# Performance work log

Hardware: AMD Instinct MI355X
Metric: run time of the kernel (lower is better)

Reference implementation:

```python
import jax, jax.numpy as jnp
import numpy as np

FEAT_DIM = 256
DEPTH = 2
N = 8192


def setup_inputs() -> dict:
    key = jax.random.key(0)
    ks = jax.random.split(key, 5)
    bd = 1.0 / FEAT_DIM
    X = jax.random.normal(ks[0], (N, FEAT_DIM), dtype=jnp.float32)
    coefs = jax.random.normal(ks[1], (N,), dtype=jnp.float32)
    linear = jax.random.uniform(ks[2], (DEPTH, FEAT_DIM), minval=-bd, maxval=bd, dtype=jnp.float32)
    dirv = jax.random.uniform(ks[3], (DEPTH, FEAT_DIM), minval=-bd, maxval=bd, dtype=jnp.float32)
    feat = jax.random.uniform(ks[4], (DEPTH, FEAT_DIM), minval=-bd, maxval=bd, dtype=jnp.float32)
    return {"X": X, "coefs": coefs, "linear": linear, "dirv": dirv, "feat": feat}


def reference(X, coefs, linear, dirv, feat):
    # coefs is unused: the torch forward returns before the coef_embed branch.
    emb = X
    n = X.shape[0]
    for i in range(linear.shape[0]):  # depth: small fixed loop
        # torch: emb3[j,a,k] = linear[a]*emb[j,k]; q = sum_a feat[a]*emb3 = (feat.linear)*emb
        a = jnp.dot(feat[i], linear[i])
        b = jnp.dot(dirv[i], linear[i])
        q = a * emb                      # [N, F]
        k = b * emb                      # [N, F]
        k_norm = k / jnp.linalg.norm(k)  # global Frobenius norm, as torch.norm(k)
        inner = jnp.sum(q * k_norm, axis=-1)            # [N]
        scale = jnp.where(inner <= 0, inner, 0.0)       # inner * (inner<=0)
        emb = q - scale[:, None] * k_norm
        # graph_block: X_up[i] = X[i] + (X@X[i]) @ (X - X[i]) / N
        # == X + (S@X - rowsum(S)*X)/N with S = X X^T
        S = emb @ emb.T                                 # [N, N]
        emb = emb + (S @ emb - jnp.sum(S, axis=1, keepdims=True) * emb) / n
    out = jnp.mean(emb @ emb.T, axis=-1)[:-1]           # [N-1]
    return out
```

## Files before the change

kernel.cpp:

```cpp
#include <hip/hip_runtime.h>
#include <math.h>

constexpr int NROW = 8192;
constexpr int FD   = 256;
constexpr int NZ   = 16;

typedef unsigned short u16;
typedef __attribute__((ext_vector_type(8))) short short8;
typedef __attribute__((ext_vector_type(4))) float f32x4;


__device__ __forceinline__ float f_of(float nj, float A, float B, float AB) {
    float inner = AB * nj;
    return A - (inner <= 0.f ? inner : 0.f) * B;
}
__device__ __forceinline__ float wred(float s) {
    #pragma unroll
    for (int off = 32; off; off >>= 1) s += __shfl_xor(s, off);
    return s;
}
__device__ __forceinline__ float dot4(float4 a, float4 b) {
    return a.x*b.x + a.y*b.y + a.z*b.z + a.w*b.w;
}
__device__ __forceinline__ u16 f2bf(float x) {
    unsigned int u = __float_as_uint(x);
    u = (u + 0x7FFFu + ((u >> 16) & 1u)) >> 16;
    return (u16)u;
}

__global__ void k_norm(const float* __restrict__ in, float* __restrict__ nrm,
                       float* __restrict__ fpart) {
    __shared__ float bs[4];
    int wave = threadIdx.x >> 6, lane = threadIdx.x & 63;
    int row = blockIdx.x * 4 + wave;
    const float4 v = *(const float4*)&in[(size_t)row * FD + lane * 4];
    float s = wred(dot4(v, v));
    if (lane == 0) { nrm[row] = s; bs[wave] = s; }
    __syncthreads();
    if (threadIdx.x == 0) fpart[blockIdx.x] = bs[0] + bs[1] + bs[2] + bs[3];
}

__global__ void __launch_bounds__(256, 2)
k_prep(const float* __restrict__ X, const float* __restrict__ nrm0,
       const float* __restrict__ fpart, const float* __restrict__ linear,
       const float* __restrict__ dirv, const float* __restrict__ feat,
       float* __restrict__ scal, float* __restrict__ f0,
       u16* __restrict__ Rbf, u16* __restrict__ Rt, float* __restrict__ cpart) {
    __shared__ u16 T[64][264];
    __shared__ float cred[4][256];
    __shared__ float l[256];
    __shared__ float ff[64];
    __shared__ float sdot[4];
    const int tid = threadIdx.x;
    const int r0 = blockIdx.x * 64;
    if (tid < 64) {
        for (int i = 0; i < 2; ++i) {
            float pa = 0.f, pb = 0.f;
            for (int k = tid; k < FD; k += 64) {
                float ll = linear[i*FD + k];
                pa += feat[i*FD + k] * ll;
                pb += dirv[i*FD + k] * ll;
            }
            pa = wred(pa); pb = wred(pb);
            if (tid == 0) { sdot[i] = pa; sdot[2 + i] = pb; }
        }
    }
    float s = 0.f;
    #pragma unroll
    for (int k = 0; k < 8; ++k) s += fpart[tid + k * 256];
    l[tid] = s;
    __syncthreads();
    for (int off = 128; off; off >>= 1) {
        if (tid < off) l[tid] += l[tid + off];
        __syncthreads();
    }
    const float F2 = l[0];
    const float a = sdot[0], b = sdot[2];
    const float sb = (b > 0.f) ? 1.f : ((b < 0.f) ? -1.f : 0.f);
    const float B = sb / sqrtf(F2);
    const float A = a, AB = a * B;
    if (blockIdx.x == 0 && tid == 0) {
        scal[0] = sdot[0]; scal[1] = sdot[1]; scal[2] = sdot[2]; scal[3] = sdot[3];
        scal[4] = A; scal[5] = B; scal[6] = AB; scal[7] = F2;
    }
    if (tid < 64) {
        float f = f_of(nrm0[r0 + tid], A, B, AB);
        ff[tid] = f;
        f0[r0 + tid] = f;
    }
    __syncthreads();
    const int cg = (tid & 63) * 4;
    const int rg = tid >> 6;
    float4 csum = make_float4(0.f, 0.f, 0.f, 0.f);
    for (int i = 0; i < 16; ++i) {
        int row = rg * 16 + i;
        float4 v = *(const float4*)&X[(size_t)(r0 + row) * FD + cg];
        float f = ff[row];
        v.x *= f; v.y *= f; v.z *= f; v.w *= f;
        csum.x += v.x; csum.y += v.y; csum.z += v.z; csum.w += v.w;
        unsigned lo = (unsigned)f2bf(v.x) | ((unsigned)f2bf(v.y) << 16);
        unsigned hi = (unsigned)f2bf(v.z) | ((unsigned)f2bf(v.w) << 16);
        uint2 pk = make_uint2(lo, hi);
        *(uint2*)&Rbf[(size_t)(r0 + row) * FD + cg] = pk;
        *(uint2*)&T[row][cg] = pk;
    }
    *(float4*)&cred[rg][cg] = csum;
    __syncthreads();
    cpart[(size_t)blockIdx.x * FD + tid] =
        cred[0][tid] + cred[1][tid] + cred[2][tid] + cred[3][tid];
    const int c = tid;
    #pragma unroll
    for (int ch = 0; ch < 8; ++ch) {
        unsigned w0 = (unsigned)T[ch*8+0][c] | ((unsigned)T[ch*8+1][c] << 16);
        unsigned w1 = (unsigned)T[ch*8+2][c] | ((unsigned)T[ch*8+3][c] << 16);
        unsigned w2 = (unsigned)T[ch*8+4][c] | ((unsigned)T[ch*8+5][c] << 16);
        unsigned w3 = (unsigned)T[ch*8+6][c] | ((unsigned)T[ch*8+7][c] << 16);
        uint4 o = make_uint4(w0, w1, w2, w3);
        *(uint4*)&Rt[(size_t)c * NROW + r0 + ch * 8] = o;
    }
}

__global__ void __launch_bounds__(256, 2)
k_gram(const u16* __restrict__ Rt, float* __restrict__ Gp) {
    const int bi = blockIdx.x, bj = blockIdx.y, z = blockIdx.z;
    const int tid = threadIdx.x, w = tid >> 6, lane = tid & 63;
    const int l15 = lane & 15, quad = lane >> 4;
    const int m0 = bi * 64 + (w & 1) * 32;
    const int n0 = bj * 64 + (w >> 1) * 32;
    const size_t kbase = (size_t)z * 512 + quad * 8;
    const u16* am0 = Rt + (size_t)(m0 + l15) * NROW + kbase;
    const u16* am1 = am0 + (size_t)16 * NROW;
    const u16* bn0 = Rt + (size_t)(n0 + l15) * NROW + kbase;
    const u16* bn1 = bn0 + (size_t)16 * NROW;
    f32x4 acc[2][2] = {};
    #pragma unroll
    for (int s = 0; s < 16; ++s) {
        int ko = s * 32;
        short8 a0 = *(const short8*)(am0 + ko);
        short8 a1 = *(const short8*)(am1 + ko);
        short8 b0 = *(const short8*)(bn0 + ko);
        short8 b1 = *(const short8*)(bn1 + ko);
        acc[0][0] = __builtin_amdgcn_mfma_f32_16x16x32_bf16(a0, b0, acc[0][0], 0, 0, 0);
        acc[0][1] = __builtin_amdgcn_mfma_f32_16x16x32_bf16(a0, b1, acc[0][1], 0, 0, 0);
        acc[1][0] = __builtin_amdgcn_mfma_f32_16x16x32_bf16(a1, b0, acc[1][0], 0, 0, 0);
        acc[1][1] = __builtin_amdgcn_mfma_f32_16x16x32_bf16(a1, b1, acc[1][1], 0, 0, 0);
    }
    float* gz = Gp + (size_t)z * (FD * FD);
    #pragma unroll
    for (int mi = 0; mi < 2; ++mi)
        #pragma unroll
        for (int ni = 0; ni < 2; ++ni)
            #pragma unroll
            for (int r = 0; r < 4; ++r)
                gz[(size_t)(m0 + mi*16 + quad*4 + r) * FD + n0 + ni*16 + l15] =
                    acc[mi][ni][r];
}

__global__ void k_gred(const float* __restrict__ Gp, u16* __restrict__ Gbf) {
    size_t e0 = (size_t)blockIdx.x * 256 + threadIdx.x;
    float s = 0.f;
    #pragma unroll
    for (int z = 0; z < NZ; ++z) s += Gp[(size_t)z * (FD * FD) + e0];
    Gbf[e0] = f2bf(s);
}

__global__ void __launch_bounds__(256, 2)
k_apply(const float* __restrict__ X, const u16* __restrict__ Rbf,
        const u16* __restrict__ Gbf, const float* __restrict__ f0,
        const float* __restrict__ cpart, float* __restrict__ emb,
        float* __restrict__ nrm1, float* __restrict__ fpart1,
        float* __restrict__ cpart1, float* __restrict__ wpart1) {
    __shared__ float Sl[32][260];
    __shared__ float csh[FD];
    __shared__ float u0s[32], ffs[32], nrs[32];
    __shared__ float nw8[32][8];
    const int tid = threadIdx.x, w = tid >> 6, lane = tid & 63;
    const int l15 = lane & 15, quad = lane >> 4;
    const int r0 = blockIdx.x * 32;

    {
        float s = 0.f;
        #pragma unroll 8
        for (int b = 0; b < 128; ++b) s += cpart[(size_t)b * FD + tid];
        csh[tid] = s;
    }
    if (tid < 32) ffs[tid] = f0[r0 + tid];
    __syncthreads();
    #pragma unroll
    for (int jj = 0; jj < 8; ++jj) {
        int row = w * 8 + jj;
        float4 xv = *(const float4*)&X[(size_t)(r0 + row) * FD + lane * 4];
        float4 cv = *(const float4*)&csh[lane * 4];
        float t = wred(dot4(xv, cv));
        if (lane == 0) u0s[row] = ffs[row] * t;
    }
    const u16* ap0 = Rbf + (size_t)(r0 + l15) * FD + quad * 8;
    const u16* ap1 = ap0 + (size_t)16 * FD;
    const int n0w = w * 64;
    const u16* bp = Gbf + (size_t)(n0w + l15) * FD + quad * 8;
    f32x4 acc[2][4] = {};
    #pragma unroll
    for (int s = 0; s < 8; ++s) {
        int ko = s * 32;
        short8 a0 = *(const short8*)(ap0 + ko);
        short8 a1 = *(const short8*)(ap1 + ko);
        short8 b0 = *(const short8*)(bp + ko);
        short8 b1 = *(const short8*)(bp + 16 * FD + ko);
        short8 b2 = *(const short8*)(bp + 32 * FD + ko);
        short8 b3 = *(const short8*)(bp + 48 * FD + ko);
        acc[0][0] = __builtin_amdgcn_mfma_f32_16x16x32_bf16(a0, b0, acc[0][0], 0, 0, 0);
        acc[0][1] = __builtin_amdgcn_mfma_f32_16x16x32_bf16(a0, b1, acc[0][1], 0, 0, 0);
        acc[0][2] = __builtin_amdgcn_mfma_f32_16x16x32_bf16(a0, b2, acc[0][2], 0, 0, 0);
        acc[0][3] = __builtin_amdgcn_mfma_f32_16x16x32_bf16(a0, b3, acc[0][3], 0, 0, 0);
        acc[1][0] = __builtin_amdgcn_mfma_f32_16x16x32_bf16(a1, b0, acc[1][0], 0, 0, 0);
        acc[1][1] = __builtin_amdgcn_mfma_f32_16x16x32_bf16(a1, b1, acc[1][1], 0, 0, 0);
        acc[1][2] = __builtin_amdgcn_mfma_f32_16x16x32_bf16(a1, b2, acc[1][2], 0, 0, 0);
        acc[1][3] = __builtin_amdgcn_mfma_f32_16x16x32_bf16(a1, b3, acc[1][3], 0, 0, 0);
    }
    #pragma unroll
    for (int mi = 0; mi < 2; ++mi)
        #pragma unroll
        for (int ni = 0; ni < 4; ++ni)
            #pragma unroll
            for (int r = 0; r < 4; ++r)
                Sl[mi*16 + quad*4 + r][n0w + ni*16 + l15] = acc[mi][ni][r];
    __syncthreads();
    const float invN = 1.0f / NROW;
    float er[32];
    float csum = 0.f;
    #pragma unroll
    for (int j = 0; j < 32; ++j) {
        float x = X[(size_t)(r0 + j) * FD + tid];
        float rv = ffs[j] * x;
        float e = rv + (Sl[j][tid] - u0s[j] * rv) * invN;
        emb[(size_t)(r0 + j) * FD + tid] = e;
        er[j] = e;
        csum += e;
        Sl[j][tid] = e * e;
    }
    __syncthreads();
    {
        int row = tid & 31, q = tid >> 5;
        float pn = 0.f;
        #pragma unroll
        for (int i = 0; i < 32; ++i) pn += Sl[row][q * 32 + i];
        nw8[row][q] = pn;
    }
    __syncthreads();
    if (tid < 32) {
        float nn = 0.f;
        #pragma unroll
        for (int q = 0; q < 8; ++q) nn += nw8[tid][q];
        nrm1[r0 + tid] = nn;
        nrs[tid] = nn;
    }
    __syncthreads();
    float wsum = 0.f;
    #pragma unroll
    for (int j = 0; j < 32; ++j) wsum += nrs[j] * er[j];
    cpart1[(size_t)blockIdx.x * FD + tid] = csum;
    wpart1[(size_t)blockIdx.x * FD + tid] = wsum;
    if (tid == 0) {
        float fp = 0.f;
        #pragma unroll
        for (int j = 0; j < 32; ++j) fp += nrs[j];
        fpart1[blockIdx.x] = fp;
    }
}

__device__ __forceinline__ void red1_scal(const float* fpart1, const float* scal,
                                          float* l, float& A, float& B, float& AB,
                                          float& kap) {
    int tid = threadIdx.x;
    l[tid] = fpart1[tid];
    __syncthreads();
    for (int off = 128; off; off >>= 1) {
        if (tid < off) l[tid] += l[tid + off];
        __syncthreads();
    }
    float F2 = l[0];
    float a = scal[1], b = scal[3];
    float sb = (b > 0.f) ? 1.f : ((b < 0.f) ? -1.f : 0.f);
    B = sb / sqrtf(F2);
    A = a; AB = a * B;
    kap = (AB <= 0.f) ? AB * B : 0.f;
    __syncthreads();
}

__global__ void k_sv(const float* __restrict__ fpart1, const float* __restrict__ scal,
                     const float* __restrict__ cpart1, const float* __restrict__ wpart1,
                     float* __restrict__ svec) {
    __shared__ float l[256];
    float A1, B1, AB1, kap;
    red1_scal(fpart1, scal, l, A1, B1, AB1, kap);
    int tid = threadIdx.x;
    int col = blockIdx.x * 4 + (tid >> 6);
    int lane = tid & 63;
    float cs = 0.f, wsm = 0.f;
    #pragma unroll
    for (int b = lane; b < 256; b += 64) {
        cs  += cpart1[(size_t)b * FD + col];
        wsm += wpart1[(size_t)b * FD + col];
    }
    #pragma unroll
    for (int off = 32; off; off >>= 1) {
        cs  += __shfl_down(cs, off);
        wsm += __shfl_down(wsm, off);
    }
    if (lane == 0) svec[col] = A1 * cs - kap * wsm;
}

__global__ void k_uv(const float* __restrict__ emb, const float* __restrict__ nrm1,
                     const float* __restrict__ scal, const float* __restrict__ fpart1,
                     const float* __restrict__ svec, float* __restrict__ u,
                     float* __restrict__ vpart) {
    __shared__ float l[256];
    __shared__ float ssh[FD];
    __shared__ float uf[16];
    float A, B, AB, kap;
    red1_scal(fpart1, scal, l, A, B, AB, kap);
    int tid = threadIdx.x;
    int r0 = blockIdx.x * 16;
    ssh[tid] = svec[tid];
    __syncthreads();
    const int wave = tid >> 6, lane = tid & 63;
    float4 sv = *(const float4*)&ssh[lane*4];
    #pragma unroll
    for (int jj = 0; jj < 4; ++jj) {
        int row = r0 + wave * 4 + jj;
        float4 ev = *(const float4*)&emb[(size_t)row * FD + lane*4];
        float s = wred(dot4(ev, sv));
        if (lane == 0) {
            float f = A - kap * nrm1[row];
            float uj = f * s;
            u[row] = uj;
            uf[wave*4 + jj] = uj * f;
        }
    }
    __syncthreads();
    float vp = 0.f;
    #pragma unroll
    for (int j = 0; j < 16; ++j)
        vp += uf[j] * emb[(size_t)(r0 + j) * FD + tid];
    vpart[(size_t)blockIdx.x * FD + tid] = vp;
}

__global__ void k_vred(const float* __restrict__ part, float* __restrict__ vec) {
    int tid = threadIdx.x;
    int col = blockIdx.x * 4 + (tid >> 6);
    int lane = tid & 63;
    float s = 0.f;
    #pragma unroll
    for (int b = 0; b < 8; ++b) s += part[(size_t)(b * 64 + lane) * FD + col];
    #pragma unroll
    for (int off = 32; off; off >>= 1) s += __shfl_down(s, off);
    if (lane == 0) vec[col] = s;
}

__global__ void k_out(const float* __restrict__ emb, const float* __restrict__ nrm1,
                      const float* __restrict__ scal, const float* __restrict__ fpart1,
                      const float* __restrict__ vvec, const float* __restrict__ u,
                      float* __restrict__ out) {
    __shared__ float l[256];
    __shared__ float vsh[FD];
    float A, B, AB, kap;
    red1_scal(fpart1, scal, l, A, B, AB, kap);
    int tid = threadIdx.x;
    int r0 = blockIdx.x * 16;
    vsh[tid] = vvec[tid];
    __syncthreads();
    const int wave = tid >> 6, lane = tid & 63;
    const float invN = 1.0f / NROW;
    float4 vv = *(const float4*)&vsh[lane*4];
    #pragma unroll
    for (int jj = 0; jj < 4; ++jj) {
        int row = r0 + wave * 4 + jj;
        float4 ev = *(const float4*)&emb[(size_t)row * FD + lane*4];
        float s = wred(dot4(ev, vv));
        if (lane == 0 && row < NROW - 1) {
            float f = A - kap * nrm1[row];
            float uj = u[row];
            out[row] = (uj + (f * s - uj * uj) * invN) * invN;
        }
    }
}

extern "C" void kernel_launch(void* const* d_in, const int* in_sizes, int n_in,
                              void* d_out, int out_size, void* d_ws, size_t ws_size,
                              hipStream_t stream) {
    const float* X      = (const float*)d_in[0];
    const float* linear = (const float*)d_in[2];
    const float* dirv   = (const float*)d_in[3];
    const float* feat   = (const float*)d_in[4];
    float* out = (float*)d_out;

    char* ws = (char*)d_ws;
    float* scal   = (float*)(ws + 0);
    float* nrm0   = (float*)(ws + 4096);
    float* nrm1   = (float*)(ws + 36864);
    float* fpart  = (float*)(ws + 69632);
    float* fpart1 = (float*)(ws + 77824);
    float* svec   = (float*)(ws + 78848);
    float* vvec   = (float*)(ws + 79872);
    float* u      = (float*)(ws + 81920);
    float* f0     = (float*)(ws + 114688);
    float* cpart  = (float*)(ws + 147456);
    u16*   Gbf    = (u16*)  (ws + 278528);
    float* cpart1 = (float*)(ws + 409600);
    float* wpart1 = (float*)(ws + 671744);
    float* vpart  = (float*)(ws + 933888);
    u16*   Rbf    = (u16*)  (ws + 2097152);
    u16*   Rt     = (u16*)  (ws + 6291456);
    float* Gp     = (float*)(ws + 10485760);
    float* emb    = (float*)(ws + 18874368);

    k_norm<<<NROW/4, 256, 0, stream>>>(X, nrm0, fpart);
    k_prep<<<128, 256, 0, stream>>>(X, nrm0, fpart, linear, dirv, feat,
                                    scal, f0, Rbf, Rt, cpart);
    k_gram<<<dim3(4,4,NZ), 256, 0, stream>>>(Rt, Gp);
    k_gred<<<256, 256, 0, stream>>>(Gp, Gbf);
    k_apply<<<256, 256, 0, stream>>>(X, Rbf, Gbf, f0, cpart, emb, nrm1,
                                     fpart1, cpart1, wpart1);
    k_sv<<<64, 256, 0, stream>>>(fpart1, scal, cpart1, wpart1, svec);
    k_uv<<<NROW/16, 256, 0, stream>>>(emb, nrm1, scal, fpart1, svec, u, vpart);
    k_vred<<<64, 256, 0, stream>>>(vpart, vvec);
    k_out<<<NROW/16, 256, 0, stream>>>(emb, nrm1, scal, fpart1, vvec, u, out);
}
```

Measured before the change: 126.0 us.

## Fuse tail kernels into cooperative grid kernel and halve row tiles

Replaces the separate k_uv, k_vred and k_out kernels with a single cooperative kernel. It keeps each block's emb rows in registers across two grid-wide syncs, so emb is read once and two launches disappear. k_prep and k_apply now use half-size row tiles with twice as many blocks, which raises parallelism. The cpart reduction is pre-reduced in k_gred so each k_apply block sums 16 partials instead of 128. The cooperative launch depends on all 512 blocks being co-resident, and grid syncs add their own latency.

```diff
diff --git a/kernel.cpp b/kernel.cpp
--- a/kernel.cpp
+++ b/kernel.cpp
@@ -1,5 +1,8 @@
 #include <hip/hip_runtime.h>
+#include <hip/hip_cooperative_groups.h>
 #include <math.h>
+
+namespace cgr = cooperative_groups;
 
 constexpr int NROW = 8192;
 constexpr int FD   = 256;
@@ -46,13 +49,13 @@
        const float* __restrict__ dirv, const float* __restrict__ feat,
        float* __restrict__ scal, float* __restrict__ f0,
        u16* __restrict__ Rbf, u16* __restrict__ Rt, float* __restrict__ cpart) {
-    __shared__ u16 T[64][264];
+    __shared__ u16 T[32][264];
     __shared__ float cred[4][256];
     __shared__ float l[256];
-    __shared__ float ff[64];
+    __shared__ float ff[32];
     __shared__ float sdot[4];
     const int tid = threadIdx.x;
-    const int r0 = blockIdx.x * 64;
+    const int r0 = blockIdx.x * 32;
     if (tid < 64) {
         for (int i = 0; i < 2; ++i) {
             float pa = 0.f, pb = 0.f;
@@ -83,34 +86,35 @@
         scal[0] = sdot[0]; scal[1] = sdot[1]; scal[2] = sdot[2]; scal[3] = sdot[3];
         scal[4] = A; scal[5] = B; scal[6] = AB; scal[7] = F2;
     }
-    if (tid < 64) {
+    if (tid < 32) {
         float f = f_of(nrm0[r0 + tid], A, B, AB);
         ff[tid] = f;
         f0[r0 + tid] = f;
     }
     __syncthreads();
-    const int cg = (tid & 63) * 4;
+    const int cg0 = (tid & 63) * 4;
     const int rg = tid >> 6;
     float4 csum = make_float4(0.f, 0.f, 0.f, 0.f);
-    for (int i = 0; i < 16; ++i) {
-        int row = rg * 16 + i;
-        float4 v = *(const float4*)&X[(size_t)(r0 + row) * FD + cg];
+    #pragma unroll
+    for (int i = 0; i < 8; ++i) {
+        int row = rg * 8 + i;
+        float4 v = *(const float4*)&X[(size_t)(r0 + row) * FD + cg0];
         float f = ff[row];
         v.x *= f; v.y *= f; v.z *= f; v.w *= f;
         csum.x += v.x; csum.y += v.y; csum.z += v.z; csum.w += v.w;
         unsigned lo = (unsigned)f2bf(v.x) | ((unsigned)f2bf(v.y) << 16);
         unsigned hi = (unsigned)f2bf(v.z) | ((unsigned)f2bf(v.w) << 16);
         uint2 pk = make_uint2(lo, hi);
-        *(uint2*)&Rbf[(size_t)(r0 + row) * FD + cg] = pk;
-        *(uint2*)&T[row][cg] = pk;
-    }
-    *(float4*)&cred[rg][cg] = csum;
+        *(uint2*)&Rbf[(size_t)(r0 + row) * FD + cg0] = pk;
+        *(uint2*)&T[row][cg0] = pk;
+    }
+    *(float4*)&cred[rg][cg0] = csum;
     __syncthreads();
     cpart[(size_t)blockIdx.x * FD + tid] =
         cred[0][tid] + cred[1][tid] + cred[2][tid] + cred[3][tid];
     const int c = tid;
     #pragma unroll
-    for (int ch = 0; ch < 8; ++ch) {
+    for (int ch = 0; ch < 4; ++ch) {
         unsigned w0 = (unsigned)T[ch*8+0][c] | ((unsigned)T[ch*8+1][c] << 16);
         unsigned w1 = (unsigned)T[ch*8+2][c] | ((unsigned)T[ch*8+3][c] << 16);
         unsigned w2 = (unsigned)T[ch*8+4][c] | ((unsigned)T[ch*8+5][c] << 16);
@@ -156,80 +160,80 @@
                     acc[mi][ni][r];
 }
 
-__global__ void k_gred(const float* __restrict__ Gp, u16* __restrict__ Gbf) {
+__global__ void k_gred(const float* __restrict__ Gp, u16* __restrict__ Gbf,
+                       const float* __restrict__ cpart, float* __restrict__ cpart2) {
     size_t e0 = (size_t)blockIdx.x * 256 + threadIdx.x;
     float s = 0.f;
     #pragma unroll
     for (int z = 0; z < NZ; ++z) s += Gp[(size_t)z * (FD * FD) + e0];
     Gbf[e0] = f2bf(s);
+    if (blockIdx.x < 16) {
+        float c = 0.f;
+        #pragma unroll
+        for (int k = 0; k < 16; ++k)
+            c += cpart[(size_t)(blockIdx.x * 16 + k) * FD + threadIdx.x];
+        cpart2[(size_t)blockIdx.x * FD + threadIdx.x] = c;
+    }
 }
 
 __global__ void __launch_bounds__(256, 2)
 k_apply(const float* __restrict__ X, const u16* __restrict__ Rbf,
         const u16* __restrict__ Gbf, const float* __restrict__ f0,
-        const float* __restrict__ cpart, float* __restrict__ emb,
+        const float* __restrict__ cpart2, float* __restrict__ emb,
         float* __restrict__ nrm1, float* __restrict__ fpart1,
         float* __restrict__ cpart1, float* __restrict__ wpart1) {
-    __shared__ float Sl[32][260];
+    __shared__ float Sl[16][260];
     __shared__ float csh[FD];
-    __shared__ float u0s[32], ffs[32], nrs[32];
-    __shared__ float nw8[32][8];
+    __shared__ float u0s[16], ffs[16], nrs[16];
+    __shared__ float nw16[16][16];
     const int tid = threadIdx.x, w = tid >> 6, lane = tid & 63;
     const int l15 = lane & 15, quad = lane >> 4;
-    const int r0 = blockIdx.x * 32;
+    const int r0 = blockIdx.x * 16;
 
     {
         float s = 0.f;
-        #pragma unroll 8
-        for (int b = 0; b < 128; ++b) s += cpart[(size_t)b * FD + tid];
+        #pragma unroll
+        for (int g = 0; g < 16; ++g) s += cpart2[(size_t)g * FD + tid];
         csh[tid] = s;
     }
-    if (tid < 32) ffs[tid] = f0[r0 + tid];
-    __syncthreads();
-    #pragma unroll
-    for (int jj = 0; jj < 8; ++jj) {
-        int row = w * 8 + jj;
+    if (tid < 16) ffs[tid] = f0[r0 + tid];
+    __syncthreads();
+    #pragma unroll
+    for (int jj = 0; jj < 4; ++jj) {
+        int row = w * 4 + jj;
         float4 xv = *(const float4*)&X[(size_t)(r0 + row) * FD + lane * 4];
         float4 cv = *(const float4*)&csh[lane * 4];
         float t = wred(dot4(xv, cv));
         if (lane == 0) u0s[row] = ffs[row] * t;
     }
-    const u16* ap0 = Rbf + (size_t)(r0 + l15) * FD + quad * 8;
-    const u16* ap1 = ap0 + (size_t)16 * FD;
+    const u16* ap = Rbf + (size_t)(r0 + l15) * FD + quad * 8;
     const int n0w = w * 64;
     const u16* bp = Gbf + (size_t)(n0w + l15) * FD + quad * 8;
-    f32x4 acc[2][4] = {};
+    f32x4 acc[4] = {};
     #pragma unroll
     for (int s = 0; s < 8; ++s) {
         int ko = s * 32;
-        short8 a0 = *(const short8*)(ap0 + ko);
-        short8 a1 = *(const short8*)(ap1 + ko);
+        short8 a0 = *(const short8*)(ap + ko);
         short8 b0 = *(const short8*)(bp + ko);
         short8 b1 = *(const short8*)(bp + 16 * FD + ko);
         short8 b2 = *(const short8*)(bp + 32 * FD + ko);
         short8 b3 = *(const short8*)(bp + 48 * FD + ko);
-        acc[0][0] = __builtin_amdgcn_mfma_f32_16x16x32_bf16(a0, b0, acc[0][0], 0, 0, 0);
-        acc[0][1] = __builtin_amdgcn_mfma_f32_16x16x32_bf16(a0, b1, acc[0][1], 0, 0, 0);
-        acc[0][2] = __builtin_amdgcn_mfma_f32_16x16x32_bf16(a0, b2, acc[0][2], 0, 0, 0);
-        acc[0][3] = __builtin_amdgcn_mfma_f32_16x16x32_bf16(a0, b3, acc[0][3], 0, 0, 0);
-        acc[1][0] = __builtin_amdgcn_mfma_f32_16x16x32_bf16(a1, b0, acc[1][0], 0, 0, 0);
-        acc[1][1] = __builtin_amdgcn_mfma_f32_16x16x32_bf16(a1, b1, acc[1][1], 0, 0, 0);
-        acc[1][2] = __builtin_amdgcn_mfma_f32_16x16x32_bf16(a1, b2, acc[1][2], 0, 0, 0);
-        acc[1][3] = __builtin_amdgcn_mfma_f32_16x16x32_bf16(a1, b3, acc[1][3], 0, 0, 0);
-    }
-    #pragma unroll
-    for (int mi = 0; mi < 2; ++mi)
-        #pragma unroll
-        for (int ni = 0; ni < 4; ++ni)
-            #pragma unroll
-            for (int r = 0; r < 4; ++r)
-                Sl[mi*16 + quad*4 + r][n0w + ni*16 + l15] = acc[mi][ni][r];
+        acc[0] = __builtin_amdgcn_mfma_f32_16x16x32_bf16(a0, b0, acc[0], 0, 0, 0);
+        acc[1] = __builtin_amdgcn_mfma_f32_16x16x32_bf16(a0, b1, acc[1], 0, 0, 0);
+        acc[2] = __builtin_amdgcn_mfma_f32_16x16x32_bf16(a0, b2, acc[2], 0, 0, 0);
+        acc[3] = __builtin_amdgcn_mfma_f32_16x16x32_bf16(a0, b3, acc[3], 0, 0, 0);
+    }
+    #pragma unroll
+    for (int ni = 0; ni < 4; ++ni)
+        #pragma unroll
+        for (int r = 0; r < 4; ++r)
+            Sl[quad*4 + r][n0w + ni*16 + l15] = acc[ni][r];
     __syncthreads();
     const float invN = 1.0f / NROW;
-    float er[32];
+    float er[16];
     float csum = 0.f;
     #pragma unroll
-    for (int j = 0; j < 32; ++j) {
+    for (int j = 0; j < 16; ++j) {
         float x = X[(size_t)(r0 + j) * FD + tid];
         float rv = ffs[j] * x;
         float e = rv + (Sl[j][tid] - u0s[j] * rv) * invN;
@@ -240,30 +244,30 @@
     }
     __syncthreads();
     {
-        int row = tid & 31, q = tid >> 5;
+        int row = tid & 15, q = tid >> 4;
         float pn = 0.f;
         #pragma unroll
-        for (int i = 0; i < 32; ++i) pn += Sl[row][q * 32 + i];
-        nw8[row][q] = pn;
-    }
-    __syncthreads();
-    if (tid < 32) {
+        for (int i = 0; i < 16; ++i) pn += Sl[row][q * 16 + i];
+        nw16[row][q] = pn;
+    }
+    __syncthreads();
+    if (tid < 16) {
         float nn = 0.f;
         #pragma unroll
-        for (int q = 0; q < 8; ++q) nn += nw8[tid][q];
+        for (int q = 0; q < 16; ++q) nn += nw16[tid][q];
         nrm1[r0 + tid] = nn;
         nrs[tid] = nn;
     }
     __syncthreads();
     float wsum = 0.f;
     #pragma unroll
-    for (int j = 0; j < 32; ++j) wsum += nrs[j] * er[j];
+    for (int j = 0; j < 16; ++j) wsum += nrs[j] * er[j];
     cpart1[(size_t)blockIdx.x * FD + tid] = csum;
     wpart1[(size_t)blockIdx.x * FD + tid] = wsum;
     if (tid == 0) {
         float fp = 0.f;
         #pragma unroll
-        for (int j = 0; j < 32; ++j) fp += nrs[j];
+        for (int j = 0; j < 16; ++j) fp += nrs[j];
         fpart1[blockIdx.x] = fp;
     }
 }
@@ -272,7 +276,7 @@
                                           float* l, float& A, float& B, float& AB,
                                           float& kap) {
     int tid = threadIdx.x;
-    l[tid] = fpart1[tid];
+    l[tid] = fpart1[tid] + fpart1[tid + 256];
     __syncthreads();
     for (int off = 128; off; off >>= 1) {
         if (tid < off) l[tid] += l[tid + off];
@@ -289,7 +293,7 @@
 
 __global__ void k_sv(const float* __restrict__ fpart1, const float* __restrict__ scal,
                      const float* __restrict__ cpart1, const float* __restrict__ wpart1,
-                     float* __restrict__ svec) {
+                     float* __restrict__ svec, float* __restrict__ scal2) {
     __shared__ float l[256];
     float A1, B1, AB1, kap;
     red1_scal(fpart1, scal, l, A1, B1, AB1, kap);
@@ -298,7 +302,7 @@
     int lane = tid & 63;
     float cs = 0.f, wsm = 0.f;
     #pragma unroll
-    for (int b = lane; b < 256; b += 64) {
+    for (int b = lane; b < 512; b += 64) {
         cs  += cpart1[(size_t)b * FD + col];
         wsm += wpart1[(size_t)b * FD + col];
     }
@@ -308,79 +312,68 @@
         wsm += __shfl_down(wsm, off);
     }
     if (lane == 0) svec[col] = A1 * cs - kap * wsm;
-}
-
-__global__ void k_uv(const float* __restrict__ emb, const float* __restrict__ nrm1,
-                     const float* __restrict__ scal, const float* __restrict__ fpart1,
-                     const float* __restrict__ svec, float* __restrict__ u,
-                     float* __restrict__ vpart) {
-    __shared__ float l[256];
-    __shared__ float ssh[FD];
-    __shared__ float uf[16];
-    float A, B, AB, kap;
-    red1_scal(fpart1, scal, l, A, B, AB, kap);
-    int tid = threadIdx.x;
-    int r0 = blockIdx.x * 16;
-    ssh[tid] = svec[tid];
-    __syncthreads();
-    const int wave = tid >> 6, lane = tid & 63;
-    float4 sv = *(const float4*)&ssh[lane*4];
-    #pragma unroll
-    for (int jj = 0; jj < 4; ++jj) {
-        int row = r0 + wave * 4 + jj;
-        float4 ev = *(const float4*)&emb[(size_t)row * FD + lane*4];
-        float s = wred(dot4(ev, sv));
-        if (lane == 0) {
-            float f = A - kap * nrm1[row];
-            float uj = f * s;
-            u[row] = uj;
-            uf[wave*4 + jj] = uj * f;
-        }
+    if (blockIdx.x == 0 && tid == 0) { scal2[0] = A1; scal2[1] = kap; }
+}
+
+__global__ void __launch_bounds__(256, 2)
+k_tailc(const float* __restrict__ emb, const float* __restrict__ nrm1,
+        const float* __restrict__ scal2, const float* __restrict__ svec,
+        float* __restrict__ vpart, float* __restrict__ vvec,
+        float* __restrict__ out) {
+    cgr::grid_group gg = cgr::this_grid();
+    __shared__ float red[4][16];
+    __shared__ float u_sh[16], uf_sh[16], f_sh[16];
+    const int tid = threadIdx.x, w = tid >> 6, lane = tid & 63;
+    const int bid = blockIdx.x;
+    const int r0 = bid * 16;
+    const float A1 = scal2[0], kap = scal2[1];
+    if (tid < 16) f_sh[tid] = A1 - kap * nrm1[r0 + tid];
+    const float svt = svec[tid];
+    float er[16];
+    #pragma unroll
+    for (int j = 0; j < 16; ++j) er[j] = emb[(size_t)(r0 + j) * FD + tid];
+    #pragma unroll
+    for (int j = 0; j < 16; ++j) {
+        float v = wred(er[j] * svt);
+        if (lane == 0) red[w][j] = v;
+    }
+    __syncthreads();
+    if (tid < 16) {
+        float s = red[0][tid] + red[1][tid] + red[2][tid] + red[3][tid];
+        float f = f_sh[tid];
+        float uj = f * s;
+        u_sh[tid] = uj; uf_sh[tid] = uj * f;
     }
     __syncthreads();
     float vp = 0.f;
     #pragma unroll
-    for (int j = 0; j < 16; ++j)
-        vp += uf[j] * emb[(size_t)(r0 + j) * FD + tid];
-    vpart[(size_t)blockIdx.x * FD + tid] = vp;
-}
-
-__global__ void k_vred(const float* __restrict__ part, float* __restrict__ vec) {
-    int tid = threadIdx.x;
-    int col = blockIdx.x * 4 + (tid >> 6);
-    int lane = tid & 63;
-    float s = 0.f;
-    #pragma unroll
-    for (int b = 0; b < 8; ++b) s += part[(size_t)(b * 64 + lane) * FD + col];
-    #pragma unroll
-    for (int off = 32; off; off >>= 1) s += __shfl_down(s, off);
-    if (lane == 0) vec[col] = s;
-}
-
-__global__ void k_out(const float* __restrict__ emb, const float* __restrict__ nrm1,
-                      const float* __restrict__ scal, const float* __restrict__ fpart1,
-                      const float* __restrict__ vvec, const float* __restrict__ u,
-                      float* __restrict__ out) {
-    __shared__ float l[256];
-    __shared__ float vsh[FD];
-    float A, B, AB, kap;
-    red1_scal(fpart1, scal, l, A, B, AB, kap);
-    int tid = threadIdx.x;
-    int r0 = blockIdx.x * 16;
-    vsh[tid] = vvec[tid];
-    __syncthreads();
-    const int wave = tid >> 6, lane = tid & 63;
-    const float invN = 1.0f / NROW;
-    float4 vv = *(const float4*)&vsh[lane*4];
-    #pragma unroll
-    for (int jj = 0; jj < 4; ++jj) {
-        int row = r0 + wave * 4 + jj;
-        float4 ev = *(const float4*)&emb[(size_t)row * FD + lane*4];
-        float s = wred(dot4(ev, vv));
-        if (lane == 0 && row < NROW - 1) {
-            float f = A - kap * nrm1[row];
-            float uj = u[row];
-            out[row] = (uj + (f * s - uj * uj) * invN) * invN;
+    for (int j = 0; j < 16; ++j) vp += uf_sh[j] * er[j];
+    vpart[(size_t)bid * FD + tid] = vp;
+    gg.sync();
+    if (bid < 64) {
+        int col = bid * 4 + (tid >> 6);
+        float s = 0.f;
+        #pragma unroll
+        for (int b2 = 0; b2 < 8; ++b2) s += vpart[(size_t)(b2 * 64 + lane) * FD + col];
+        #pragma unroll
+        for (int off = 32; off; off >>= 1) s += __shfl_down(s, off);
+        if (lane == 0) vvec[col] = s;
+    }
+    gg.sync();
+    const float vvt = vvec[tid];
+    #pragma unroll
+    for (int j = 0; j < 16; ++j) {
+        float v = wred(er[j] * vvt);
+        if (lane == 0) red[w][j] = v;
+    }
+    __syncthreads();
+    if (tid < 16) {
+        int row = r0 + tid;
+        if (row < NROW - 1) {
+            float s2 = red[0][tid] + red[1][tid] + red[2][tid] + red[3][tid];
+            float f = f_sh[tid], uj = u_sh[tid];
+            const float invN = 1.0f / NROW;
+            out[row] = (uj + (f * s2 - uj * uj) * invN) * invN;
         }
     }
 }
@@ -396,33 +389,34 @@
 
     char* ws = (char*)d_ws;
     float* scal   = (float*)(ws + 0);
-    float* nrm0   = (float*)(ws + 4096);
-    float* nrm1   = (float*)(ws + 36864);
-    float* fpart  = (float*)(ws + 69632);
-    float* fpart1 = (float*)(ws + 77824);
-    float* svec   = (float*)(ws + 78848);
-    float* vvec   = (float*)(ws + 79872);
-    float* u      = (float*)(ws + 81920);
-    float* f0     = (float*)(ws + 114688);
-    float* cpart  = (float*)(ws + 147456);
-    u16*   Gbf    = (u16*)  (ws + 278528);
-    float* cpart1 = (float*)(ws + 409600);
-    float* wpart1 = (float*)(ws + 671744);
-    float* vpart  = (float*)(ws + 933888);
+    float* scal2  = (float*)(ws + 128);
+    float* fpart  = (float*)(ws + 4096);
+    float* nrm0   = (float*)(ws + 12288);
+    float* nrm1   = (float*)(ws + 45056);
+    float* f0     = (float*)(ws + 77824);
+    float* fpart1 = (float*)(ws + 110592);
+    float* svec   = (float*)(ws + 112640);
+    float* vvec   = (float*)(ws + 113664);
+    float* cpart2 = (float*)(ws + 114688);
+    float* cpart  = (float*)(ws + 131072);
+    float* cpart1 = (float*)(ws + 393216);
+    float* wpart1 = (float*)(ws + 917504);
+    float* vpart  = (float*)(ws + 1441792);
+    u16*   Gbf    = (u16*)  (ws + 1966080);
     u16*   Rbf    = (u16*)  (ws + 2097152);
     u16*   Rt     = (u16*)  (ws + 6291456);
     float* Gp     = (float*)(ws + 10485760);
-    float* emb    = (float*)(ws + 18874368);
+    float* emb    = (float*)(ws + 14680064);
 
     k_norm<<<NROW/4, 256, 0, stream>>>(X, nrm0, fpart);
-    k_prep<<<128, 256, 0, stream>>>(X, nrm0, fpart, linear, dirv, feat,
+    k_prep<<<256, 256, 0, stream>>>(X, nrm0, fpart, linear, dirv, feat,
                                     scal, f0, Rbf, Rt, cpart);
     k_gram<<<dim3(4,4,NZ), 256, 0, stream>>>(Rt, Gp);
-    k_gred<<<256, 256, 0, stream>>>(Gp, Gbf);
-    k_apply<<<256, 256, 0, stream>>>(X, Rbf, Gbf, f0, cpart, emb, nrm1,
+    k_gred<<<256, 256, 0, stream>>>(Gp, Gbf, cpart, cpart2);
+    k_apply<<<512, 256, 0, stream>>>(X, Rbf, Gbf, f0, cpart2, emb, nrm1,
                                      fpart1, cpart1, wpart1);
-    k_sv<<<64, 256, 0, stream>>>(fpart1, scal, cpart1, wpart1, svec);
-    k_uv<<<NROW/16, 256, 0, stream>>>(emb, nrm1, scal, fpart1, svec, u, vpart);
-    k_vred<<<64, 256, 0, stream>>>(vpart, vvec);
-    k_out<<<NROW/16, 256, 0, stream>>>(emb, nrm1, scal, fpart1, vvec, u, out);
-}
+    k_sv<<<64, 256, 0, stream>>>(fpart1, scal, cpart1, wpart1, svec, scal2);
+    void* targs[] = {(void*)&emb, (void*)&nrm1, (void*)&scal2, (void*)&svec,
+                     (void*)&vpart, (void*)&vvec, (void*)&out};
+    hipLaunchCooperativeKernel(k_tailc, dim3(512), dim3(256), targs, 0, stream);
+}
```

Result: slower. 242.6 us (+92.5%).
